# Kernel tuning notes

Hardware: AMD Instinct MI355X
Metric: run time of the kernel (lower is better)

## Reference

```python
import jax, jax.numpy as jnp
import numpy as np

N = 16384        # num_variables
C = 512          # number of budget constraints
K = 64           # variables per constraint (uniform constraint_sizes)
STRIDE = 32      # overlapping windows -> every variable has degree 2
BATCH = 64
BUDGET = 8.0     # budgets[i]
MAX_ITER = 25    # ADMM / AD3 iterations
RHO = 1.0        # penalty parameter
BISECT = 25      # bisection steps for the budget projection threshold


def setup_inputs() -> dict:
    key = jax.random.key(0)
    scores = jax.random.normal(key, (BATCH, N), dtype=jnp.float32)
    # constraint_sets: constraint c covers variables [c*STRIDE, c*STRIDE+K) mod N
    base = (np.arange(C)[:, None] * STRIDE + np.arange(K)[None, :]) % N
    constraint_idx = jnp.asarray(base, dtype=jnp.int32)  # [C, K]
    return {"scores": scores, "constraint_idx": constraint_idx}


def _proj_budget(a, budget):
    """Project rows a[..., K] onto {z in [0,1]^K : sum(z) <= budget}."""
    z0 = jnp.clip(a, 0.0, 1.0)
    feasible = jnp.sum(z0, -1, keepdims=True) <= budget
    # bisection for tau with sum(clip(a - tau, 0, 1)) == budget
    a_sg = jax.lax.stop_gradient(a)
    lo = jnp.min(a_sg, -1, keepdims=True) - 1.0
    hi = jnp.max(a_sg, -1, keepdims=True)
    for _ in range(BISECT):  # fixed small algorithmic loop
        mid = 0.5 * (lo + hi)
        s = jnp.sum(jnp.clip(a_sg - mid, 0.0, 1.0), -1, keepdims=True)
        lo = jnp.where(s > budget, mid, lo)
        hi = jnp.where(s > budget, hi, mid)
    tau0 = 0.5 * (lo + hi)
    # one implicit (Newton) correction so tau is differentiable in a
    active = ((a_sg - tau0 > 0.0) & (a_sg - tau0 < 1.0)).astype(a.dtype)
    n_act = jnp.maximum(jnp.sum(active, -1, keepdims=True), 1.0)
    g = jnp.sum(jnp.clip(a - tau0, 0.0, 1.0), -1, keepdims=True) - budget
    tau = tau0 + g / n_act
    z_proj = jnp.clip(a - tau, 0.0, 1.0)
    return jnp.where(feasible, z0, z_proj)


def _forward(scores, constraint_idx):
    B, n_vars = scores.shape
    idx = constraint_idx  # [C, K]
    deg = jnp.zeros((n_vars,), scores.dtype).at[idx.reshape(-1)].add(1.0)
    deg_safe = jnp.maximum(deg, 1.0)

    def u_update(z, lam):
        # u = (theta + A^T(rho*z - lam)) / (rho * deg), boxed to [0,1]
        msg = RHO * z - lam                                   # [B,C,K]
        t = jnp.zeros_like(scores).at[:, idx].add(msg)        # A^T scatter
        u = (scores + t) / (RHO * deg_safe)
        u = jnp.clip(u, 0.0, 1.0)
        # unconstrained variables: LP optimum is the indicator of theta > 0
        return jnp.where(deg > 0.0, u, (scores > 0.0).astype(scores.dtype))

    def step(carry, _):
        z, lam = carry
        u = u_update(z, lam)
        Au = u[:, idx]                                        # gather [B,C,K]
        z_new = _proj_budget(Au + lam / RHO, BUDGET)
        lam_new = lam + RHO * (Au - z_new)
        return (z_new, lam_new), None

    z0 = jnp.zeros((B, idx.shape[0], idx.shape[1]), scores.dtype)
    lam0 = jnp.zeros_like(z0)
    (z, lam), _ = jax.lax.scan(step, (z0, lam0), None, length=MAX_ITER)
    return u_update(z, lam)


def reference(scores, constraint_idx):
    return _forward(scores, constraint_idx)
```

## Files before the change

kernel.cpp:

```cpp
#include <hip/hip_runtime.h>
#include <math.h>


#define NGLOB   16384
#define KD      64
#define MAXIT   25
#define NBIS    9
#define BUDGETF 8.0f
#define CHUNK   128
#define HALO    25
#define NCREAL  (CHUNK + 2*HALO)
#define NROWP   192
#define NTHREADS 768
#define MSGROWS (NROWP + 2)
#define RS4     17
#define OFF4    (MSGROWS * RS4)

typedef float v4f __attribute__((ext_vector_type(4)));
typedef float v2f __attribute__((ext_vector_type(2)));

__device__ __forceinline__ float clip01(float x) {
    return __builtin_amdgcn_fmed3f(x, 0.0f, 1.0f);
}
__device__ __forceinline__ v4f clipv(v4f x) {
    v4f r;
    r.x = clip01(x.x); r.y = clip01(x.y); r.z = clip01(x.z); r.w = clip01(x.w);
    return r;
}
__device__ __forceinline__ v4f minv(v4f a, v4f b) {
    v4f r; r.x=fminf(a.x,b.x); r.y=fminf(a.y,b.y); r.z=fminf(a.z,b.z); r.w=fminf(a.w,b.w); return r;
}
__device__ __forceinline__ v4f maxv(v4f a, v4f b) {
    v4f r; r.x=fmaxf(a.x,b.x); r.y=fmaxf(a.y,b.y); r.z=fmaxf(a.z,b.z); r.w=fmaxf(a.w,b.w); return r;
}
__device__ __forceinline__ float sum16(v4f a, v4f b, v4f c, v4f d) {
    v4f t = (a + b) + (c + d);
    v2f u = t.xy + t.zw;
    return u.x + u.y;
}
__device__ __forceinline__ float min16(v4f a, v4f b, v4f c, v4f d) {
    v4f t = minv(minv(a, b), minv(c, d));
    return fminf(fminf(t.x, t.y), fminf(t.z, t.w));
}
__device__ __forceinline__ float max16(v4f a, v4f b, v4f c, v4f d) {
    v4f t = maxv(maxv(a, b), maxv(c, d));
    return fmaxf(fmaxf(t.x, t.y), fmaxf(t.z, t.w));
}

template<int CTRL>
__device__ __forceinline__ float dpp_mv(float x) {
    union U { float f; int i; } s, r;
    s.f = x;
    r.i = __builtin_amdgcn_update_dpp(0, s.i, CTRL, 0xf, 0xf, true);
    return r.f;
}
__device__ __forceinline__ float g4_sum(float x) {
    x += dpp_mv<0xB1>(x);
    x += dpp_mv<0x4E>(x);
    return x;
}
__device__ __forceinline__ float g4_min(float x) {
    x = fminf(x, dpp_mv<0xB1>(x));
    x = fminf(x, dpp_mv<0x4E>(x));
    return x;
}
__device__ __forceinline__ float g4_max(float x) {
    x = fmaxf(x, dpp_mv<0xB1>(x));
    x = fmaxf(x, dpp_mv<0x4E>(x));
    return x;
}

__global__ void __launch_bounds__(NTHREADS, 3)
lpsmap_kernel(const float* __restrict__ scores, float* __restrict__ out) {
    __shared__ float msg[2 * OFF4 * 4];
    v4f* msg4 = (v4f*)msg;

    const int tid  = threadIdx.x;
    const int wid  = tid >> 6;
    const int lane = tid & 63;
    const int g    = lane >> 2;
    const int l4   = lane & 3;
    const int khi  = l4 >> 1;
    const int lc   = l4 & 1;
    const int b    = blockIdx.x >> 2;
    const int c0v  = (blockIdx.x & 3) * (CHUNK * 32);
    const float* sb = scores + b * NGLOB;

    for (int i = tid; i < 2 * OFF4; i += NTHREADS)
        msg4[i] = v4f{0.0f, 0.0f, 0.0f, 0.0f};

    const int rr = wid * 16 + g;
    const int i1 = (rr + khi + 1) * RS4 + 4 * lc;
    const int i2 = (rr + khi) * RS4 + 8 + 4 * lc;
    const int iw = (rr + 1) * RS4 + 4 * l4;
    const int inb = (l4 < 2) ? i2 : i1;

    v4f sch[4], lam[4], av[4], msgr[4];
    {
        const int off = (c0v - HALO * 32 + rr * 32 + 16 * l4 + NGLOB) & (NGLOB - 1);
        const v4f* gp = (const v4f*)(sb + off);
        #pragma unroll
        for (int q = 0; q < 4; ++q) {
            sch[q]  = gp[q] * 0.5f;
            lam[q]  = v4f{0.0f, 0.0f, 0.0f, 0.0f};
            msgr[q] = v4f{0.0f, 0.0f, 0.0f, 0.0f};
        }
    }

    __syncthreads();

    int roff = 0;
    #pragma unroll 1
    for (int it = 0; it < MAXIT; ++it) {
        const v4f* mr = msg4 + roff;
        v4f*       mw = msg4 + (roff ^ OFF4);

        #pragma unroll
        for (int q = 0; q < 4; ++q) {
            v4f nb = mr[inb + q];
            v4f u  = clipv((msgr[q] + nb) * 0.5f + sch[q]);
            av[q]  = u + lam[q];
        }

        float lo = g4_min(min16(av[0], av[1], av[2], av[3])) - 1.0f;
        float hi = g4_max(max16(av[0], av[1], av[2], av[3]));
        float s_lo = 64.0f;
        float s_hi = 0.0f;

        #pragma unroll 1
        for (int j = 0; j < NBIS; ++j) {
            float mid = 0.5f * (lo + hi);
            float s = g4_sum(sum16(clipv(av[0] - mid), clipv(av[1] - mid),
                                   clipv(av[2] - mid), clipv(av[3] - mid)));
            bool gt = s > BUDGETF;
            lo   = gt ? mid : lo;
            hi   = gt ? hi  : mid;
            s_lo = gt ? s   : s_lo;
            s_hi = gt ? s_hi : s;
        }

        {
            float tau = lo + (s_lo - BUDGETF) * (hi - lo)
                             * __builtin_amdgcn_rcpf(s_lo - s_hi);
            tau = fmaxf(tau, 0.0f);
            #pragma unroll
            for (int q = 0; q < 4; ++q) {
                v4f z   = clipv(av[q] - tau);
                lam[q]  = av[q] - z;
                msgr[q] = 2.0f * z - av[q];
                mw[iw + q] = msgr[q];
            }
        }
        roff ^= OFF4;
        __syncthreads();
    }

    if (tid < CHUNK * 32 / 8) {
        const v4f* mr = msg4 + roff;
        const int j   = tid * 8;
        const int vl  = HALO * 32 + j;
        const int rrl = vl >> 5;
        const int cq  = (vl & 31) >> 2;
        v4f m1a = mr[(rrl + 1) * RS4 + cq],   m1b = mr[(rrl + 1) * RS4 + cq + 1];
        v4f m2a = mr[rrl * RS4 + 8 + cq],     m2b = mr[rrl * RS4 + 8 + cq + 1];
        const v4f* gp = (const v4f*)(sb + c0v + j);
        v4f u0 = clipv((gp[0] + m1a + m2a) * 0.5f);
        v4f u1 = clipv((gp[1] + m1b + m2b) * 0.5f);
        v4f* op = (v4f*)(out + (size_t)b * NGLOB + c0v + j);
        op[0] = u0;
        op[1] = u1;
    }
}

extern "C" void kernel_launch(void* const* d_in, const int* in_sizes, int n_in,
                              void* d_out, int out_size, void* d_ws, size_t ws_size,
                              hipStream_t stream) {
    const float* scores = (const float*)d_in[0];
    float* out = (float*)d_out;
    dim3 grid(64 * 4);
    dim3 block(NTHREADS);
    lpsmap_kernel<<<grid, block, 0, stream>>>(scores, out);
}
```

Baseline: 117.1 us.

## Process two constraint rows per thread group with half the threads per block

Each 4-lane group now handles two constraint rows (NPACK=2) held in registers, so the block drops from 768 to 384 threads and the bisection steps for both rows are interleaved for instruction-level parallelism. The final output is computed from the register-held messages and scores instead of reloading scores from global memory. This cuts warps per block and barrier participants but doubles register use per thread, which lowers occupancy (launch bounds set to 1 block per CU).

```diff
diff --git a/kernel.cpp b/kernel.cpp
--- a/kernel.cpp
+++ b/kernel.cpp
@@ -9,9 +9,10 @@
 #define BUDGETF 8.0f
 #define CHUNK   128
 #define HALO    25
-#define NCREAL  (CHUNK + 2*HALO)
+#define NPACK   2
+#define NW      6
+#define NTHREADS 384
 #define NROWP   192
-#define NTHREADS 768
 #define MSGROWS (NROWP + 2)
 #define RS4     17
 #define OFF4    (MSGROWS * RS4)
@@ -70,7 +71,7 @@
     return x;
 }
 
-__global__ void __launch_bounds__(NTHREADS, 3)
+__global__ void __launch_bounds__(NTHREADS, 1)
 lpsmap_kernel(const float* __restrict__ scores, float* __restrict__ out) {
     __shared__ float msg[2 * OFF4 * 4];
     v4f* msg4 = (v4f*)msg;
@@ -89,21 +90,26 @@
     for (int i = tid; i < 2 * OFF4; i += NTHREADS)
         msg4[i] = v4f{0.0f, 0.0f, 0.0f, 0.0f};
 
-    const int rr = wid * 16 + g;
-    const int i1 = (rr + khi + 1) * RS4 + 4 * lc;
-    const int i2 = (rr + khi) * RS4 + 8 + 4 * lc;
-    const int iw = (rr + 1) * RS4 + 4 * l4;
-    const int inb = (l4 < 2) ? i2 : i1;
-
-    v4f sch[4], lam[4], av[4], msgr[4];
-    {
-        const int off = (c0v - HALO * 32 + rr * 32 + 16 * l4 + NGLOB) & (NGLOB - 1);
+    int rr[NPACK], inb[NPACK], iw[NPACK];
+    #pragma unroll
+    for (int p = 0; p < NPACK; ++p) {
+        rr[p] = wid * 32 + p * 16 + g;
+        const int i1 = (rr[p] + khi + 1) * RS4 + 4 * lc;
+        const int i2 = (rr[p] + khi) * RS4 + 8 + 4 * lc;
+        inb[p] = (l4 < 2) ? i2 : i1;
+        iw[p]  = (rr[p] + 1) * RS4 + 4 * l4;
+    }
+
+    v4f sch[NPACK][4], lam[NPACK][4], av[NPACK][4], msgr[NPACK][4];
+    #pragma unroll
+    for (int p = 0; p < NPACK; ++p) {
+        const int off = (c0v - HALO * 32 + rr[p] * 32 + 16 * l4 + NGLOB) & (NGLOB - 1);
         const v4f* gp = (const v4f*)(sb + off);
         #pragma unroll
         for (int q = 0; q < 4; ++q) {
-            sch[q]  = gp[q] * 0.5f;
-            lam[q]  = v4f{0.0f, 0.0f, 0.0f, 0.0f};
-            msgr[q] = v4f{0.0f, 0.0f, 0.0f, 0.0f};
+            sch[p][q]  = gp[q] * 0.5f;
+            lam[p][q]  = v4f{0.0f, 0.0f, 0.0f, 0.0f};
+            msgr[p][q] = v4f{0.0f, 0.0f, 0.0f, 0.0f};
         }
     }
 
@@ -116,59 +122,70 @@
         v4f*       mw = msg4 + (roff ^ OFF4);
 
         #pragma unroll
-        for (int q = 0; q < 4; ++q) {
-            v4f nb = mr[inb + q];
-            v4f u  = clipv((msgr[q] + nb) * 0.5f + sch[q]);
-            av[q]  = u + lam[q];
-        }
-
-        float lo = g4_min(min16(av[0], av[1], av[2], av[3])) - 1.0f;
-        float hi = g4_max(max16(av[0], av[1], av[2], av[3]));
-        float s_lo = 64.0f;
-        float s_hi = 0.0f;
+        for (int p = 0; p < NPACK; ++p) {
+            #pragma unroll
+            for (int q = 0; q < 4; ++q) {
+                v4f nb = mr[inb[p] + q];
+                v4f u  = clipv((msgr[p][q] + nb) * 0.5f + sch[p][q]);
+                av[p][q] = u + lam[p][q];
+            }
+        }
+
+        float lo[NPACK], hi[NPACK], s_lo[NPACK], s_hi[NPACK];
+        #pragma unroll
+        for (int p = 0; p < NPACK; ++p) {
+            lo[p] = g4_min(min16(av[p][0], av[p][1], av[p][2], av[p][3])) - 1.0f;
+            hi[p] = g4_max(max16(av[p][0], av[p][1], av[p][2], av[p][3]));
+            s_lo[p] = 64.0f;
+            s_hi[p] = 0.0f;
+        }
 
         #pragma unroll 1
         for (int j = 0; j < NBIS; ++j) {
-            float mid = 0.5f * (lo + hi);
-            float s = g4_sum(sum16(clipv(av[0] - mid), clipv(av[1] - mid),
-                                   clipv(av[2] - mid), clipv(av[3] - mid)));
-            bool gt = s > BUDGETF;
-            lo   = gt ? mid : lo;
-            hi   = gt ? hi  : mid;
-            s_lo = gt ? s   : s_lo;
-            s_hi = gt ? s_hi : s;
-        }
-
-        {
-            float tau = lo + (s_lo - BUDGETF) * (hi - lo)
-                             * __builtin_amdgcn_rcpf(s_lo - s_hi);
+            #pragma unroll
+            for (int p = 0; p < NPACK; ++p) {
+                float mid = 0.5f * (lo[p] + hi[p]);
+                float s = g4_sum(sum16(clipv(av[p][0] - mid), clipv(av[p][1] - mid),
+                                       clipv(av[p][2] - mid), clipv(av[p][3] - mid)));
+                bool gt = s > BUDGETF;
+                lo[p]   = gt ? mid : lo[p];
+                hi[p]   = gt ? hi[p] : mid;
+                s_lo[p] = gt ? s : s_lo[p];
+                s_hi[p] = gt ? s_hi[p] : s;
+            }
+        }
+
+        #pragma unroll
+        for (int p = 0; p < NPACK; ++p) {
+            float tau = lo[p] + (s_lo[p] - BUDGETF) * (hi[p] - lo[p])
+                               * __builtin_amdgcn_rcpf(s_lo[p] - s_hi[p]);
             tau = fmaxf(tau, 0.0f);
             #pragma unroll
             for (int q = 0; q < 4; ++q) {
-                v4f z   = clipv(av[q] - tau);
-                lam[q]  = av[q] - z;
-                msgr[q] = 2.0f * z - av[q];
-                mw[iw + q] = msgr[q];
+                v4f z      = clipv(av[p][q] - tau);
+                lam[p][q]  = av[p][q] - z;
+                msgr[p][q] = 2.0f * z - av[p][q];
+                mw[iw[p] + q] = msgr[p][q];
             }
         }
         roff ^= OFF4;
         __syncthreads();
     }
 
-    if (tid < CHUNK * 32 / 8) {
+    {
         const v4f* mr = msg4 + roff;
-        const int j   = tid * 8;
-        const int vl  = HALO * 32 + j;
-        const int rrl = vl >> 5;
-        const int cq  = (vl & 31) >> 2;
-        v4f m1a = mr[(rrl + 1) * RS4 + cq],   m1b = mr[(rrl + 1) * RS4 + cq + 1];
-        v4f m2a = mr[rrl * RS4 + 8 + cq],     m2b = mr[rrl * RS4 + 8 + cq + 1];
-        const v4f* gp = (const v4f*)(sb + c0v + j);
-        v4f u0 = clipv((gp[0] + m1a + m2a) * 0.5f);
-        v4f u1 = clipv((gp[1] + m1b + m2b) * 0.5f);
-        v4f* op = (v4f*)(out + (size_t)b * NGLOB + c0v + j);
-        op[0] = u0;
-        op[1] = u1;
+        #pragma unroll
+        for (int p = 0; p < NPACK; ++p) {
+            if (l4 < 2 && rr[p] >= HALO && rr[p] < HALO + CHUNK) {
+                v4f* op = (v4f*)(out + (size_t)b * NGLOB + c0v
+                                 + (rr[p] - HALO) * 32 + 16 * l4);
+                #pragma unroll
+                for (int q = 0; q < 4; ++q) {
+                    v4f nb = mr[inb[p] + q];
+                    op[q] = clipv((msgr[p][q] + nb) * 0.5f + sch[p][q]);
+                }
+            }
+        }
     }
 }
 
```

Result: slower. 149.8 us (+27.9%).
